# Kernel tuning notes

Measured on AMD Instinct MI355X. Metric: run time of the kernel, lower is better.

The kernel has to match this reference:

```python
import jax, jax.numpy as jnp
import numpy as np
from jax import lax

VOCAB = 32000
D_MODEL = 1024
N_LAYERS = 4
D_STATE = 8
D_CONV = 4
EXPAND = 2
D_INNER = EXPAND * D_MODEL          # 2048
DT_RANK = (D_MODEL + 15) // 16      # 64
B, L = 2, 1024


def setup_inputs() -> dict:
    key = jax.random.key(0)
    ks = jax.random.split(key, 20)
    s = 0.02
    inp = {
        "input_ids": jax.random.randint(ks[0], (B, L), 0, VOCAB, dtype=jnp.int32),
        "embed": jax.random.normal(ks[1], (VOCAB, D_MODEL), jnp.float32) * s,
        "in_proj_w": jax.random.normal(ks[2], (N_LAYERS, 2 * D_INNER, D_MODEL), jnp.float32) * s,
        "conv_w": jax.random.normal(ks[3], (N_LAYERS, D_INNER, 1, D_CONV), jnp.float32) * s,
        "conv_b": jnp.zeros((N_LAYERS, D_INNER), jnp.float32),
        "x_proj_w": jax.random.normal(ks[4], (N_LAYERS, DT_RANK + 2 * D_STATE, D_INNER), jnp.float32) * s,
        "dt_proj_w": jax.random.normal(ks[5], (N_LAYERS, D_INNER, DT_RANK), jnp.float32) * s,
        "dt_proj_b": jax.random.normal(ks[6], (N_LAYERS, D_INNER), jnp.float32) * 0.1,
        "A_log": jnp.broadcast_to(jnp.log(jnp.arange(1, D_STATE + 1, dtype=jnp.float32)),
                                  (N_LAYERS, D_INNER, D_STATE)) + 0.0,
        "D": jnp.ones((N_LAYERS, D_INNER), jnp.float32),
        "out_proj_w": jax.random.normal(ks[7], (N_LAYERS, D_MODEL, D_INNER), jnp.float32) * s,
        "ln_g": jnp.ones((N_LAYERS, D_MODEL), jnp.float32),
        "ln_b": jnp.zeros((N_LAYERS, D_MODEL), jnp.float32),
        "fn_g": jnp.ones((D_MODEL,), jnp.float32),
        "fn_b": jnp.zeros((D_MODEL,), jnp.float32),
        "fc_w": jax.random.normal(ks[8], (VOCAB, D_MODEL), jnp.float32) * s,
        "fc_b": jnp.zeros((VOCAB,), jnp.float32),
    }
    return inp


def layer_norm(x, g, b, eps=1e-5):
    mu = jnp.mean(x, -1, keepdims=True)
    var = jnp.var(x, -1, keepdims=True)
    return (x - mu) * lax.rsqrt(var + eps) * g + b


def silu(x):
    return x * jax.nn.sigmoid(x)


def selective_scan(deltaA, deltaBu, C):
    # deltaA, deltaBu: (b,l,d,n); C: (b,l,n) -> y: (b,l,d)
    def step(h, inp):
        dA, dBu, c = inp
        h = dA * h + dBu                       # (b,d,n)
        y = jnp.einsum('bdn,bn->bd', h, c)
        return h, y
    h0 = jnp.zeros(deltaA.shape[:1] + deltaA.shape[2:], deltaA.dtype)
    _, ys = lax.scan(step, h0, (deltaA.transpose(1, 0, 2, 3),
                                deltaBu.transpose(1, 0, 2, 3),
                                C.transpose(1, 0, 2)))
    return ys.transpose(1, 0, 2)


def mamba_block(x, in_proj_w, conv_w, conv_b, x_proj_w, dt_proj_w, dt_proj_b, A_log, D, out_proj_w):
    # x: (b,l,d_model)
    xz = jnp.einsum('bld,ed->ble', x, in_proj_w)          # (b,l,2*di)
    xc, z = jnp.split(xz, 2, axis=-1)
    # causal depthwise conv1d, kernel D_CONV
    xc_ncl = xc.transpose(0, 2, 1)                         # (b,di,l)
    xc_ncl = lax.conv_general_dilated(
        xc_ncl, conv_w, window_strides=(1,), padding=[(D_CONV - 1, 0)],
        feature_group_count=D_INNER, dimension_numbers=('NCH', 'OIH', 'NCH'))
    xc = silu(xc_ncl.transpose(0, 2, 1) + conv_b)          # (b,l,di)
    x_dbl = jnp.einsum('bld,ed->ble', xc, x_proj_w)        # (b,l,dt_rank+2n)
    dt, Bm, Cm = jnp.split(x_dbl, [DT_RANK, DT_RANK + D_STATE], axis=-1)
    dt = jax.nn.softplus(jnp.einsum('blr,dr->bld', dt, dt_proj_w) + dt_proj_b)  # (b,l,di)
    A = -jnp.exp(A_log)                                    # (di,n)
    deltaA = jnp.exp(dt[..., None] * A)                    # (b,l,di,n)
    deltaBu = dt[..., None] * Bm[:, :, None, :] * xc[..., None]
    y = selective_scan(deltaA, deltaBu, Cm)                # (b,l,di)
    y = y + xc * D
    y = y * silu(z)
    return jnp.einsum('ble,de->bld', y, out_proj_w)


def reference(input_ids, embed, in_proj_w, conv_w, conv_b, x_proj_w, dt_proj_w,
              dt_proj_b, A_log, D, out_proj_w, ln_g, ln_b, fn_g, fn_b, fc_w, fc_b):
    x = embed[input_ids]                                   # (b,l,d)
    for i in range(N_LAYERS):
        out = mamba_block(x, in_proj_w[i], conv_w[i], conv_b[i], x_proj_w[i],
                          dt_proj_w[i], dt_proj_b[i], A_log[i], D[i], out_proj_w[i])
        x = layer_norm(out + x, ln_g[i], ln_b[i])
    x = layer_norm(x, fn_g, fn_b)
    logits = jnp.einsum('bld,vd->blv', x, fc_w) + fc_b
    return logits
```

## Files before the change

### kernel.cpp

```cpp
#include <hip/hip_runtime.h>
#include <cstddef>
#include <cstdint>

#define D_MODEL 1024
#define D_INNER 2048
#define DT_RANK 64
#define D_STATE 8
#define NLAYERS 4
#define BATCH 2
#define SEQ 1024
#define M_ROWS (BATCH*SEQ)
#define VOCAB 32000
#define XPAD 128
#define NC 32
#define LC 32
#define XSK 8

typedef __attribute__((ext_vector_type(8))) short short8;
typedef __attribute__((ext_vector_type(4))) float f32x4;

__device__ __forceinline__ float sigmoidf_(float x) { return 1.f / (1.f + __expf(-x)); }

__device__ __forceinline__ unsigned short f2bf(float f) {
    unsigned u = __float_as_uint(f);
    u += 0x7fffu + ((u >> 16) & 1u);
    return (unsigned short)(u >> 16);
}

__global__ __launch_bounds__(256) void cast_kernel(const float* __restrict__ in,
                                                   unsigned short* __restrict__ out, int n4)
{
    int i = blockIdx.x * 256 + threadIdx.x;
    if (i >= n4) return;
    float4 v = ((const float4*)in)[i];
    ushort4 o;
    o.x = f2bf(v.x); o.y = f2bf(v.y); o.z = f2bf(v.z); o.w = f2bf(v.w);
    ((ushort4*)out)[i] = o;
}

__global__ __launch_bounds__(256) void cast_pad_xproj(const float* __restrict__ in,
                                                      unsigned short* __restrict__ out)
{
    int i = blockIdx.x * 256 + threadIdx.x;
    if (i >= NLAYERS * XPAD * D_INNER / 4) return;
    int col4 = i & (D_INNER / 4 - 1);
    int row = (i >> 9) & (XPAD - 1);
    int layer = i >> 16;
    ushort4 o = {0, 0, 0, 0};
    if (row < 80) {
        float4 v = ((const float4*)(in + ((size_t)layer * 80 + row) * D_INNER))[col4];
        o.x = f2bf(v.x); o.y = f2bf(v.y); o.z = f2bf(v.z); o.w = f2bf(v.w);
    }
    ((ushort4*)out)[i] = o;
}

__global__ __launch_bounds__(256) void gather_kernel(const int* __restrict__ ids,
                                                     const float* __restrict__ embed,
                                                     float* __restrict__ x,
                                                     unsigned short* __restrict__ xb)
{
    int m = blockIdx.x;
    int t = threadIdx.x;
    int id = ids[m];
    float4 v = ((const float4*)(embed + (size_t)id * D_MODEL))[t];
    ((float4*)(x + (size_t)m * D_MODEL))[t] = v;
    ushort4 o;
    o.x = f2bf(v.x); o.y = f2bf(v.y); o.z = f2bf(v.z); o.w = f2bf(v.w);
    ((ushort4*)(xb + (size_t)m * D_MODEL))[t] = o;
}

template<int EPI>
__global__ __launch_bounds__(256) void gemm_bf16_nt(const unsigned short* __restrict__ A, int lda,
                                                    const unsigned short* __restrict__ B, int ldb,
                                                    float* __restrict__ C, int ldc,
                                                    int K, const float* __restrict__ bias)
{
    __shared__ unsigned short As[128 * 64];
    __shared__ unsigned short Bs[128 * 64];
    const int tid = threadIdx.x;

    const int gm = gridDim.x;
    const int bid = blockIdx.y * gm + blockIdx.x;
    const int q = (gm * gridDim.y) >> 3;
    const int swz = (bid & 7) * q + (bid >> 3);
    const int bm = (swz % gm) * 128, bn = (swz / gm) * 128;

    const int wid = tid >> 6, lane = tid & 63;
    const int wm = (wid >> 1) * 64, wn = (wid & 1) * 64;
    const int lrow = lane & 15, lkg = lane >> 4;

    const int srow = tid >> 3;
    const int ksrc = ((tid & 7) ^ (srow & 7)) * 8;
    const size_t kz = (size_t)blockIdx.z * K;
    const unsigned short* Ag = A + (size_t)(bm + srow) * lda + kz + ksrc;
    const unsigned short* Bg = B + (size_t)(bn + srow) * ldb + kz + ksrc;

    f32x4 acc[4][4];
    #pragma unroll
    for (int i = 0; i < 4; ++i)
        #pragma unroll
        for (int j = 0; j < 4; ++j)
            acc[i][j] = f32x4{0.f, 0.f, 0.f, 0.f};

    for (int k0 = 0; k0 < K; k0 += 64) {
        #pragma unroll
        for (int i = 0; i < 4; ++i) {
            __builtin_amdgcn_global_load_lds(
                (const __attribute__((address_space(1))) void*)(Ag + k0 + (size_t)(32 * i) * lda),
                (__attribute__((address_space(3))) void*)(As + i * 2048 + tid * 8), 16, 0, 0);
            __builtin_amdgcn_global_load_lds(
                (const __attribute__((address_space(1))) void*)(Bg + k0 + (size_t)(32 * i) * ldb),
                (__attribute__((address_space(3))) void*)(Bs + i * 2048 + tid * 8), 16, 0, 0);
        }
        __syncthreads();

        #pragma unroll
        for (int kk = 0; kk < 2; ++kk) {
            short8 af[4], bf[4];
            #pragma unroll
            for (int i = 0; i < 4; ++i) {
                int ra = wm + 16 * i + lrow;
                int pa = (kk * 4 + lkg) ^ (ra & 7);
                af[i] = *(const short8*)(As + ra * 64 + pa * 8);
                int rb = wn + 16 * i + lrow;
                int pb = (kk * 4 + lkg) ^ (rb & 7);
                bf[i] = *(const short8*)(Bs + rb * 64 + pb * 8);
            }
            #pragma unroll
            for (int i = 0; i < 4; ++i)
                #pragma unroll
                for (int j = 0; j < 4; ++j)
                    acc[i][j] = __builtin_amdgcn_mfma_f32_16x16x32_bf16(af[i], bf[j], acc[i][j], 0, 0, 0);
        }
        __syncthreads();
    }

    if (gridDim.z > 1) C += (size_t)blockIdx.z * M_ROWS * ldc;

    const int crow = bm + wm + lkg * 4;
    const int ccol = bn + wn + lrow;
    #pragma unroll
    for (int i = 0; i < 4; ++i) {
        #pragma unroll
        for (int j = 0; j < 4; ++j) {
            float bv = (EPI == 1 || EPI == 2) ? bias[ccol + 16 * j] : 0.f;
            float* Cp = C + (size_t)(crow + 16 * i) * ldc + ccol + 16 * j;
            #pragma unroll
            for (int r = 0; r < 4; ++r) {
                float v = acc[i][j][r] + bv;
                if (EPI == 1) v = (v > 20.f) ? v : log1pf(__expf(v));
                Cp[(size_t)r * ldc] = v;
            }
        }
    }
}

__global__ __launch_bounds__(256) void reduce_xdbl(const float* __restrict__ part,
                                                   float* __restrict__ xdbl,
                                                   unsigned short* __restrict__ xdbl_b)
{
    int i = blockIdx.x * 256 + threadIdx.x;
    float4 s = ((const float4*)part)[i];
    #pragma unroll
    for (int z = 1; z < XSK; ++z) {
        float4 v = ((const float4*)part)[(size_t)z * (M_ROWS * XPAD / 4) + i];
        s.x += v.x; s.y += v.y; s.z += v.z; s.w += v.w;
    }
    ((float4*)xdbl)[i] = s;
    ushort4 o;
    o.x = f2bf(s.x); o.y = f2bf(s.y); o.z = f2bf(s.z); o.w = f2bf(s.w);
    ((ushort4*)xdbl_b)[i] = o;
}

__global__ __launch_bounds__(256) void conv_silu_kernel(const float* __restrict__ xz,
                                                        const float* __restrict__ cw,
                                                        const float* __restrict__ cb,
                                                        float* __restrict__ xc,
                                                        unsigned short* __restrict__ xcb)
{
    int idx = blockIdx.x * 256 + threadIdx.x;
    int d = idx & (D_INNER - 1);
    int m = idx >> 11;
    int l = m & (SEQ - 1);
    int b = m >> 10;
    float w0 = cw[d * 4 + 0], w1 = cw[d * 4 + 1], w2 = cw[d * 4 + 2], w3 = cw[d * 4 + 3];
    float s = cb[d];
    const float* base = xz + ((size_t)b * SEQ) * (2 * D_INNER) + d;
    if (l - 3 >= 0) s += base[(size_t)(l - 3) * (2 * D_INNER)] * w0;
    if (l - 2 >= 0) s += base[(size_t)(l - 2) * (2 * D_INNER)] * w1;
    if (l - 1 >= 0) s += base[(size_t)(l - 1) * (2 * D_INNER)] * w2;
    s += base[(size_t)l * (2 * D_INNER)] * w3;
    float v = s * sigmoidf_(s);
    xc[(size_t)m * D_INNER + d] = v;
    xcb[(size_t)m * D_INNER + d] = f2bf(v);
}

__global__ __launch_bounds__(256) void scan_partial(const float* __restrict__ dt,
                                                    const float* __restrict__ xdbl,
                                                    const float* __restrict__ xc,
                                                    const float* __restrict__ A_log,
                                                    float* __restrict__ H,
                                                    float* __restrict__ P)
{
    const int tid = threadIdx.x;
    const int b = blockIdx.x & 1;
    const int c = (blockIdx.x >> 1) & (NC - 1);
    const int d = ((blockIdx.x >> 6) << 8) + tid;

    __shared__ float Bs[LC][8];
    {
        int r = tid >> 3, n = tid & 7;
        Bs[r][n] = xdbl[(size_t)(b * SEQ + c * LC + r) * XPAD + DT_RANK + n];
    }
    __syncthreads();

    float An[8];
    #pragma unroll
    for (int n = 0; n < 8; ++n) An[n] = -__expf(A_log[d * 8 + n]);
    float h[8] = {0.f,0.f,0.f,0.f,0.f,0.f,0.f,0.f};
    float p[8] = {1.f,1.f,1.f,1.f,1.f,1.f,1.f,1.f};

    const float* dtp = dt + (size_t)(b * SEQ + c * LC) * D_INNER + d;
    const float* xcp = xc + (size_t)(b * SEQ + c * LC) * D_INNER + d;
    for (int l = 0; l < LC; ++l) {
        float dtv = dtp[(size_t)l * D_INNER];
        float ux  = dtv * xcp[(size_t)l * D_INNER];
        #pragma unroll
        for (int n = 0; n < 8; ++n) {
            float dA = __expf(dtv * An[n]);
            h[n] = dA * h[n] + Bs[l][n] * ux;
            p[n] *= dA;
        }
    }
    size_t base = (size_t)((b * NC + c) * 8) * D_INNER + d;
    #pragma unroll
    for (int n = 0; n < 8; ++n) {
        H[base + (size_t)n * D_INNER] = h[n];
        P[base + (size_t)n * D_INNER] = p[n];
    }
}

__global__ __launch_bounds__(256) void scan_combine(const float* __restrict__ H,
                                                    float* __restrict__ P )
{
    int idx = blockIdx.x * 256 + threadIdx.x;
    int d = idx & (D_INNER - 1);
    int n = (idx >> 11) & 7;
    int b = idx >> 14;
    float hp = 0.f;
    for (int c = 0; c < NC; ++c) {
        size_t base = (size_t)((b * NC + c) * 8 + n) * D_INNER + d;
        float Pv = P[base], Hv = H[base];
        P[base] = hp;
        hp = Pv * hp + Hv;
    }
}

__global__ __launch_bounds__(256) void scan_final(const float* __restrict__ dt,
                                                  const float* __restrict__ xdbl,
                                                  const float* __restrict__ xc,
                                                  const float* __restrict__ xz,
                                                  const float* __restrict__ A_log,
                                                  const float* __restrict__ Dp,
                                                  const float* __restrict__ h0,
                                                  unsigned short* __restrict__ yb)
{
    const int tid = threadIdx.x;
    const int b = blockIdx.x & 1;
    const int c = (blockIdx.x >> 1) & (NC - 1);
    const int d = ((blockIdx.x >> 6) << 8) + tid;

    __shared__ float Bs[LC][8];
    __shared__ float Cs[LC][8];
    {
        int r = tid >> 3, n = tid & 7;
        size_t xrow = (size_t)(b * SEQ + c * LC + r) * XPAD;
        Bs[r][n] = xdbl[xrow + DT_RANK + n];
        Cs[r][n] = xdbl[xrow + DT_RANK + 8 + n];
    }
    __syncthreads();

    float An[8], h[8];
    size_t base = (size_t)((b * NC + c) * 8) * D_INNER + d;
    #pragma unroll
    for (int n = 0; n < 8; ++n) {
        An[n] = -__expf(A_log[d * 8 + n]);
        h[n] = h0[base + (size_t)n * D_INNER];
    }
    const float Dv = Dp[d];

    const float* dtp = dt + (size_t)(b * SEQ + c * LC) * D_INNER + d;
    const float* xcp = xc + (size_t)(b * SEQ + c * LC) * D_INNER + d;
    const float* zp  = xz + (size_t)(b * SEQ + c * LC) * (2 * D_INNER) + D_INNER + d;
    unsigned short* ybp = yb + (size_t)(b * SEQ + c * LC) * D_INNER + d;

    for (int l = 0; l < LC; ++l) {
        float dtv = dtp[(size_t)l * D_INNER];
        float xcv = xcp[(size_t)l * D_INNER];
        float zv  = zp[(size_t)l * (2 * D_INNER)];
        float ux = dtv * xcv;
        float acc = 0.f;
        #pragma unroll
        for (int n = 0; n < 8; ++n) {
            float dA = __expf(dtv * An[n]);
            h[n] = dA * h[n] + Bs[l][n] * ux;
            acc += h[n] * Cs[l][n];
        }
        float yv = (acc + xcv * Dv) * (zv * sigmoidf_(zv));
        ybp[(size_t)l * D_INNER] = f2bf(yv);
    }
}

template<bool ADD>
__global__ __launch_bounds__(256) void ln_kernel(const float* __restrict__ extra,
                                                 const float* __restrict__ xin,
                                                 float* __restrict__ xout,
                                                 unsigned short* __restrict__ xbout,
                                                 const float* __restrict__ g,
                                                 const float* __restrict__ bb)
{
    int m = blockIdx.x;
    int t = threadIdx.x;
    float4 v = ((const float4*)(xin + (size_t)m * D_MODEL))[t];
    if (ADD) {
        float4 e = ((const float4*)(extra + (size_t)m * D_MODEL))[t];
        v.x += e.x; v.y += e.y; v.z += e.z; v.w += e.w;
    }
    float s  = v.x + v.y + v.z + v.w;
    float s2 = v.x * v.x + v.y * v.y + v.z * v.z + v.w * v.w;
    for (int off = 32; off; off >>= 1) {
        s  += __shfl_down(s, off);
        s2 += __shfl_down(s2, off);
    }
    __shared__ float red[8];
    int wid = t >> 6, lane = t & 63;
    if (lane == 0) { red[wid] = s; red[wid + 4] = s2; }
    __syncthreads();
    if (t == 0) {
        float a  = red[0] + red[1] + red[2] + red[3];
        float b2 = red[4] + red[5] + red[6] + red[7];
        float mu = a * (1.f / D_MODEL);
        red[0] = mu;
        red[4] = b2 * (1.f / D_MODEL) - mu * mu;
    }
    __syncthreads();
    float mu = red[0];
    float rs = rsqrtf(red[4] + 1e-5f);
    float4 gg = ((const float4*)g)[t];
    float4 bv = ((const float4*)bb)[t];
    float4 o;
    o.x = (v.x - mu) * rs * gg.x + bv.x;
    o.y = (v.y - mu) * rs * gg.y + bv.y;
    o.z = (v.z - mu) * rs * gg.z + bv.z;
    o.w = (v.w - mu) * rs * gg.w + bv.w;
    ((float4*)(xout + (size_t)m * D_MODEL))[t] = o;
    ushort4 ob;
    ob.x = f2bf(o.x); ob.y = f2bf(o.y); ob.z = f2bf(o.z); ob.w = f2bf(o.w);
    ((ushort4*)(xbout + (size_t)m * D_MODEL))[t] = ob;
}

extern "C" void kernel_launch(void* const* d_in, const int* in_sizes, int n_in,
                              void* d_out, int out_size, void* d_ws, size_t ws_size,
                              hipStream_t stream)
{
    const int*   ids      = (const int*)d_in[0];
    const float* embed    = (const float*)d_in[1];
    const float* in_proj  = (const float*)d_in[2];
    const float* conv_w   = (const float*)d_in[3];
    const float* conv_b   = (const float*)d_in[4];
    const float* x_proj   = (const float*)d_in[5];
    const float* dt_w     = (const float*)d_in[6];
    const float* dt_b     = (const float*)d_in[7];
    const float* A_log    = (const float*)d_in[8];
    const float* Dp       = (const float*)d_in[9];
    const float* out_proj = (const float*)d_in[10];
    const float* ln_g     = (const float*)d_in[11];
    const float* ln_b     = (const float*)d_in[12];
    const float* fn_g     = (const float*)d_in[13];
    const float* fn_b     = (const float*)d_in[14];
    const float* fc_w     = (const float*)d_in[15];
    const float* fc_b     = (const float*)d_in[16];
    float* logits = (float*)d_out;

    float* ws = (float*)d_ws;
    float* x     = ws;
    float* xz    = x + (size_t)M_ROWS * D_MODEL;
    float* xc    = xz + (size_t)M_ROWS * 2 * D_INNER;
    float* xdbl  = xc + (size_t)M_ROWS * D_INNER;
    float* dtbuf = xdbl + (size_t)M_ROWS * XPAD;
    float* tmp   = dtbuf + (size_t)M_ROWS * D_INNER;
    float* xpart = tmp + (size_t)M_ROWS * D_MODEL;

    float* Hbuf = tmp;
    float* Pbuf = tmp + (size_t)BATCH * NC * D_STATE * D_INNER;

    unsigned short* xb     = (unsigned short*)(xpart + (size_t)XSK * M_ROWS * XPAD);
    unsigned short* yb     = xb + (size_t)M_ROWS * D_MODEL;
    unsigned short* xcb    = yb + (size_t)M_ROWS * D_INNER;
    unsigned short* xdbl_b = xcb + (size_t)M_ROWS * D_INNER;
    unsigned short* wb_in  = xdbl_b + (size_t)M_ROWS * XPAD;
    unsigned short* wb_out = wb_in + (size_t)NLAYERS * 2 * D_INNER * D_MODEL;
    unsigned short* wb_fc  = wb_out + (size_t)NLAYERS * D_MODEL * D_INNER;
    unsigned short* wb_x   = wb_fc + (size_t)VOCAB * D_MODEL;
    unsigned short* wb_dt  = wb_x + (size_t)NLAYERS * XPAD * D_INNER;

    {
        int n4 = NLAYERS * 2 * D_INNER * D_MODEL / 4;
        cast_kernel<<<(n4 + 255) / 256, 256, 0, stream>>>(in_proj, wb_in, n4);
        n4 = NLAYERS * D_MODEL * D_INNER / 4;
        cast_kernel<<<(n4 + 255) / 256, 256, 0, stream>>>(out_proj, wb_out, n4);
        n4 = VOCAB * D_MODEL / 4;
        cast_kernel<<<(n4 + 255) / 256, 256, 0, stream>>>(fc_w, wb_fc, n4);
        n4 = NLAYERS * D_INNER * DT_RANK / 4;
        cast_kernel<<<(n4 + 255) / 256, 256, 0, stream>>>(dt_w, wb_dt, n4);
        n4 = NLAYERS * XPAD * D_INNER / 4;
        cast_pad_xproj<<<(n4 + 255) / 256, 256, 0, stream>>>(x_proj, wb_x);
    }

    gather_kernel<<<M_ROWS, 256, 0, stream>>>(ids, embed, x, xb);

    for (int i = 0; i < NLAYERS; ++i) {
        const unsigned short* W_in_b  = wb_in + (size_t)i * 2 * D_INNER * D_MODEL;
        const unsigned short* W_out_b = wb_out + (size_t)i * D_MODEL * D_INNER;
        const unsigned short* W_x_b   = wb_x + (size_t)i * XPAD * D_INNER;
        const unsigned short* W_dt_b  = wb_dt + (size_t)i * D_INNER * DT_RANK;
        const float* cw    = conv_w + (size_t)i * D_INNER * 4;
        const float* cb    = conv_b + (size_t)i * D_INNER;
        const float* b_dt  = dt_b + (size_t)i * D_INNER;
        const float* Al    = A_log + (size_t)i * D_INNER * D_STATE;
        const float* Dl    = Dp + (size_t)i * D_INNER;
        const float* g     = ln_g + (size_t)i * D_MODEL;
        const float* bb    = ln_b + (size_t)i * D_MODEL;

        gemm_bf16_nt<0><<<dim3(M_ROWS / 128, 2 * D_INNER / 128), 256, 0, stream>>>(
            xb, D_MODEL, W_in_b, D_MODEL, xz, 2 * D_INNER, D_MODEL, nullptr);

        conv_silu_kernel<<<(M_ROWS * D_INNER) / 256, 256, 0, stream>>>(xz, cw, cb, xc, xcb);

        gemm_bf16_nt<0><<<dim3(M_ROWS / 128, 1, XSK), 256, 0, stream>>>(
            xcb, D_INNER, W_x_b, D_INNER, xpart, XPAD, D_INNER / XSK, nullptr);
        reduce_xdbl<<<(M_ROWS * XPAD / 4) / 256, 256, 0, stream>>>(xpart, xdbl, xdbl_b);

        gemm_bf16_nt<1><<<dim3(M_ROWS / 128, D_INNER / 128), 256, 0, stream>>>(
            xdbl_b, XPAD, W_dt_b, DT_RANK, dtbuf, D_INNER, DT_RANK, b_dt);

        scan_partial<<<BATCH * NC * (D_INNER / 256), 256, 0, stream>>>(
            dtbuf, xdbl, xc, Al, Hbuf, Pbuf);
        scan_combine<<<(BATCH * D_STATE * D_INNER) / 256, 256, 0, stream>>>(Hbuf, Pbuf);
        scan_final<<<BATCH * NC * (D_INNER / 256), 256, 0, stream>>>(
            dtbuf, xdbl, xc, xz, Al, Dl, Pbuf, yb);

        gemm_bf16_nt<0><<<dim3(M_ROWS / 128, D_MODEL / 128), 256, 0, stream>>>(
            yb, D_INNER, W_out_b, D_INNER, tmp, D_MODEL, D_INNER, nullptr);

        ln_kernel<true><<<M_ROWS, 256, 0, stream>>>(tmp, x, x, xb, g, bb);
    }

    ln_kernel<false><<<M_ROWS, 256, 0, stream>>>(nullptr, x, tmp, xb, fn_g, fn_b);

    gemm_bf16_nt<2><<<dim3(M_ROWS / 128, VOCAB / 128), 256, 0, stream>>>(
        xb, D_MODEL, wb_fc, D_MODEL, logits, VOCAB, D_MODEL, fc_b);
}
```

Baseline: 1.019 ms.

## Double-buffer GEMM LDS tiles with BK=32 to overlap loads and MFMA

The bf16 GEMM now uses two 128x32 LDS buffers per operand and prefetches the next K-slice with global_load_lds while computing on the current one, replacing a single 64-wide buffer with load-then-compute. The swizzle pattern is adapted to the 32-wide row layout. This aims to hide global-load latency behind MFMA work, at the cost of one barrier per 32-wide K step instead of two per 64, and a less thorough bank-conflict swizzle.

```diff
diff --git a/kernel.cpp b/kernel.cpp
--- a/kernel.cpp
+++ b/kernel.cpp
@@ -19,6 +19,9 @@
 typedef __attribute__((ext_vector_type(8))) short short8;
 typedef __attribute__((ext_vector_type(4))) float f32x4;
 
+#define GPTR(p) (const __attribute__((address_space(1))) void*)(p)
+#define LPTR(p) (__attribute__((address_space(3))) void*)(p)
+
 __device__ __forceinline__ float sigmoidf_(float x) { return 1.f / (1.f + __expf(-x)); }
 
 __device__ __forceinline__ unsigned short f2bf(float f) {
@@ -75,8 +78,8 @@
                                                     float* __restrict__ C, int ldc,
                                                     int K, const float* __restrict__ bias)
 {
-    __shared__ unsigned short As[128 * 64];
-    __shared__ unsigned short Bs[128 * 64];
+    __shared__ unsigned short As[2][128 * 32];
+    __shared__ unsigned short Bs[2][128 * 32];
     const int tid = threadIdx.x;
 
     const int gm = gridDim.x;
@@ -89,11 +92,21 @@
     const int wm = (wid >> 1) * 64, wn = (wid & 1) * 64;
     const int lrow = lane & 15, lkg = lane >> 4;
 
-    const int srow = tid >> 3;
-    const int ksrc = ((tid & 7) ^ (srow & 7)) * 8;
+    const int srow = tid >> 2;
+    const int ksrc = ((tid & 3) ^ ((srow >> 1) & 3)) * 8;
     const size_t kz = (size_t)blockIdx.z * K;
     const unsigned short* Ag = A + (size_t)(bm + srow) * lda + kz + ksrc;
     const unsigned short* Bg = B + (size_t)(bn + srow) * ldb + kz + ksrc;
+    const size_t r64a = (size_t)64 * lda;
+    const size_t r64b = (size_t)64 * ldb;
+
+#define STAGE(buf, koff)                                                                              \
+    do {                                                                                              \
+        __builtin_amdgcn_global_load_lds(GPTR(Ag + (koff)),        LPTR(&As[buf][tid * 8]), 16, 0, 0);\
+        __builtin_amdgcn_global_load_lds(GPTR(Ag + r64a + (koff)), LPTR(&As[buf][2048 + tid * 8]), 16, 0, 0);\
+        __builtin_amdgcn_global_load_lds(GPTR(Bg + (koff)),        LPTR(&Bs[buf][tid * 8]), 16, 0, 0);\
+        __builtin_amdgcn_global_load_lds(GPTR(Bg + r64b + (koff)), LPTR(&Bs[buf][2048 + tid * 8]), 16, 0, 0);\
+    } while (0)
 
     f32x4 acc[4][4];
     #pragma unroll
@@ -102,38 +115,33 @@
         for (int j = 0; j < 4; ++j)
             acc[i][j] = f32x4{0.f, 0.f, 0.f, 0.f};
 
-    for (int k0 = 0; k0 < K; k0 += 64) {
+    STAGE(0, 0);
+    __syncthreads();
+
+    int cur = 0;
+    for (int k0 = 0; k0 < K; k0 += 32) {
+        if (k0 + 32 < K) STAGE(cur ^ 1, k0 + 32);
+
+        short8 af[4], bf[4];
         #pragma unroll
         for (int i = 0; i < 4; ++i) {
-            __builtin_amdgcn_global_load_lds(
-                (const __attribute__((address_space(1))) void*)(Ag + k0 + (size_t)(32 * i) * lda),
-                (__attribute__((address_space(3))) void*)(As + i * 2048 + tid * 8), 16, 0, 0);
-            __builtin_amdgcn_global_load_lds(
-                (const __attribute__((address_space(1))) void*)(Bg + k0 + (size_t)(32 * i) * ldb),
-                (__attribute__((address_space(3))) void*)(Bs + i * 2048 + tid * 8), 16, 0, 0);
+            int ra = wm + 16 * i + lrow;
+            int pa = lkg ^ ((ra >> 1) & 3);
+            af[i] = *(const short8*)(&As[cur][ra * 32 + pa * 8]);
+            int rb = wn + 16 * i + lrow;
+            int pb = lkg ^ ((rb >> 1) & 3);
+            bf[i] = *(const short8*)(&Bs[cur][rb * 32 + pb * 8]);
         }
+        #pragma unroll
+        for (int i = 0; i < 4; ++i)
+            #pragma unroll
+            for (int j = 0; j < 4; ++j)
+                acc[i][j] = __builtin_amdgcn_mfma_f32_16x16x32_bf16(af[i], bf[j], acc[i][j], 0, 0, 0);
+
         __syncthreads();
-
-        #pragma unroll
-        for (int kk = 0; kk < 2; ++kk) {
-            short8 af[4], bf[4];
-            #pragma unroll
-            for (int i = 0; i < 4; ++i) {
-                int ra = wm + 16 * i + lrow;
-                int pa = (kk * 4 + lkg) ^ (ra & 7);
-                af[i] = *(const short8*)(As + ra * 64 + pa * 8);
-                int rb = wn + 16 * i + lrow;
-                int pb = (kk * 4 + lkg) ^ (rb & 7);
-                bf[i] = *(const short8*)(Bs + rb * 64 + pb * 8);
-            }
-            #pragma unroll
-            for (int i = 0; i < 4; ++i)
-                #pragma unroll
-                for (int j = 0; j < 4; ++j)
-                    acc[i][j] = __builtin_amdgcn_mfma_f32_16x16x32_bf16(af[i], bf[j], acc[i][j], 0, 0, 0);
-        }
-        __syncthreads();
-    }
+        cur ^= 1;
+    }
+#undef STAGE
 
     if (gridDim.z > 1) C += (size_t)blockIdx.z * M_ROWS * ldc;
 
```

New measurement: 1.017 ms. Within noise of the previous version (-0.1%).
